# Kernel tuning notes

Hardware: AMD Instinct MI355X
Metric: run time of the kernel (lower is better)

## Reference

```python
import jax, jax.numpy as jnp
import numpy as np

D_MODEL = 1024
N_HEADS = 16
D_K = D_MODEL // N_HEADS
THETA = 10000.0
MAX_SEQ_LEN = 2048


def _rope_tables(seq_len):
    pos = jnp.arange(seq_len, dtype=jnp.float32)
    inv_freq = 1.0 / (THETA ** (jnp.arange(0, D_K, 2, dtype=jnp.float32) / D_K))
    ang = pos[:, None] * inv_freq[None, :]  # [T, D_K/2]
    return jnp.cos(ang), jnp.sin(ang)


def _apply_rope(x, cos, sin):
    # x: [..., T, D_K]; cos/sin: [T, D_K/2]
    x_even = x[..., ::2]
    x_odd = x[..., 1::2]
    r_even = x_even * cos - x_odd * sin
    r_odd = x_even * sin + x_odd * cos
    out = jnp.stack([r_even, r_odd], axis=-1)  # [..., T, D_K/2, 2]
    return out.reshape(x.shape)


def setup_inputs() -> dict:
    key = jax.random.key(0)
    ks = jax.random.split(key, 5)
    std = np.sqrt(2.0 / (D_MODEL + D_MODEL))
    x = jax.random.normal(ks[0], (2, 2048, D_MODEL), dtype=jnp.float32)
    w_q = jax.random.normal(ks[1], (D_MODEL, D_MODEL), dtype=jnp.float32) * std
    w_k = jax.random.normal(ks[2], (D_MODEL, D_MODEL), dtype=jnp.float32) * std
    w_v = jax.random.normal(ks[3], (D_MODEL, D_MODEL), dtype=jnp.float32) * std
    w_o = jax.random.normal(ks[4], (D_MODEL, D_MODEL), dtype=jnp.float32) * std
    return {"x": x, "w_q": w_q, "w_k": w_k, "w_v": w_v, "w_o": w_o}


def reference(x, w_q, w_k, w_v, w_o):
    B, T, _ = x.shape
    # projections: weight stored as [d_out, d_in], y = x @ W^T
    q = jnp.einsum('btd,od->bto', x, w_q)
    k = jnp.einsum('btd,od->bto', x, w_k)
    v = jnp.einsum('btd,od->bto', x, w_v)
    # split heads: [B, T, H*Dk] -> [B, H, T, Dk]
    q = q.reshape(B, T, N_HEADS, D_K).transpose(0, 2, 1, 3)
    k = k.reshape(B, T, N_HEADS, D_K).transpose(0, 2, 1, 3)
    v = v.reshape(B, T, N_HEADS, D_K).transpose(0, 2, 1, 3)
    cos, sin = _rope_tables(T)
    q = _apply_rope(q, cos, sin)
    k = _apply_rope(k, cos, sin)
    scores = jnp.einsum('bhqd,bhkd->bhqk', q, k) / np.sqrt(D_K).astype(np.float32)
    causal = jnp.tril(jnp.ones((T, T), dtype=bool))
    scores = jnp.where(causal, scores, -jnp.inf)
    attn = jax.nn.softmax(scores, axis=-1)
    out = jnp.einsum('bhqk,bhkd->bhqd', attn, v)
    out = out.transpose(0, 2, 1, 3).reshape(B, T, D_MODEL)
    return jnp.einsum('btd,od->bto', out, w_o)
```

## Files before the change

### kernel.cpp

```cpp
#include <hip/hip_runtime.h>
#include <hip/hip_bf16.h>

typedef __bf16 bf16_t;
typedef __bf16 bf16x8 __attribute__((ext_vector_type(8)));
typedef float f32x4 __attribute__((ext_vector_type(4)));
typedef short short4v __attribute__((ext_vector_type(4)));

#define D_MODEL 1024
#define T_SEQ 2048
#define NH 16
#define DKD 64
#define X_ELEMS (4194304u)
#define W_ELEMS (1048576u)
#define Q_SCALE 0.18033688011112042f

__device__ __forceinline__ void async16(const bf16_t* g, bf16_t* l) {
    __builtin_amdgcn_global_load_lds((const __attribute__((address_space(1))) void*)g,
                                     (__attribute__((address_space(3))) void*)l, 16, 0, 0);
}

__global__ __launch_bounds__(256) void convert_kernel(
    const float* __restrict__ x, const float* __restrict__ wq,
    const float* __restrict__ wk, const float* __restrict__ wv,
    const float* __restrict__ wo,
    bf16_t* __restrict__ xb, bf16_t* __restrict__ wqb, bf16_t* __restrict__ wkb,
    bf16_t* __restrict__ wvb, bf16_t* __restrict__ wob)
{
    size_t idx = ((size_t)blockIdx.x * 256 + threadIdx.x) * 4;
    const float* src; bf16_t* dst; size_t off;
    if (idx < X_ELEMS) { src = x; dst = xb; off = idx; }
    else {
        size_t r = idx - X_ELEMS;
        unsigned w = (unsigned)(r >> 20);
        off = r & (W_ELEMS - 1);
        src = (w == 0) ? wq : (w == 1) ? wk : (w == 2) ? wv : wo;
        dst = (w == 0) ? wqb : (w == 1) ? wkb : (w == 2) ? wvb : wob;
    }
    float4 v = *(const float4*)(src + off);
    union { bf16_t b[4]; short4v s; } u;
    u.b[0] = (bf16_t)v.x; u.b[1] = (bf16_t)v.y;
    u.b[2] = (bf16_t)v.z; u.b[3] = (bf16_t)v.w;
    *(short4v*)(dst + off) = u.s;
}

__global__ __launch_bounds__(256) void rope_kernel(float* __restrict__ cost, float* __restrict__ sint)
{
    int idx = blockIdx.x * 256 + threadIdx.x;
    int t = idx >> 5, i = idx & 31;
    float inv = expf(-0.28782313662425572f * (float)i);
    float ang = (float)t * inv;
    float s, c;
    sincosf(ang, &s, &c);
    cost[idx] = c; sint[idx] = s;
}

__device__ __forceinline__ void gemm_body(
    int mode,
    const bf16_t* __restrict__ A, const bf16_t* __restrict__ W,
    bf16_t* __restrict__ qout, bf16_t* __restrict__ kout, bf16_t* __restrict__ vout,
    const float* __restrict__ cost, const float* __restrict__ sint,
    float* __restrict__ fout)
{
    __shared__ bf16_t As[128 * 64];
    __shared__ bf16_t Bs[128 * 64];
    const int tid = threadIdx.x;
    const int wave = tid >> 6, lane = tid & 63;
    const int quad = lane >> 4, l16 = lane & 15;
    const int m0 = blockIdx.x * 128;
    const int n0 = blockIdx.y * 128;
    const int wm = (wave >> 1) * 64, wn = (wave & 1) * 64;

    const bf16_t* Afrag = (mode == 2) ? Bs : As;
    const bf16_t* Bfrag = (mode == 2) ? As : Bs;
    const int aoff = (mode == 2) ? wn : wm;
    const int boff = (mode == 2) ? wm : wn;

    const f32x4 fzero = {0.f, 0.f, 0.f, 0.f};
    f32x4 acc[4][4];
    #pragma unroll
    for (int i = 0; i < 4; ++i)
        #pragma unroll
        for (int j = 0; j < 4; ++j) acc[i][j] = fzero;

    for (int k0 = 0; k0 < 1024; k0 += 64) {
        __syncthreads();
        #pragma unroll
        for (int c = 0; c < 4; ++c) {
            int G = c * 256 + tid;
            int row = G >> 3, p = G & 7;
            int go = p ^ (row & 7);
            async16(A + (size_t)(m0 + row) * 1024 + (k0 + go * 8), As + (size_t)(c * 256 + wave * 64) * 8);
            async16(W + (size_t)(n0 + row) * 1024 + (k0 + go * 8), Bs + (size_t)(c * 256 + wave * 64) * 8);
        }
        __syncthreads();
        #pragma unroll
        for (int ks = 0; ks < 2; ++ks) {
            bf16x8 af[4], bfv[4];
            #pragma unroll
            for (int mi = 0; mi < 4; ++mi) {
                int r = aoff + mi * 16 + l16;
                af[mi] = *(const bf16x8*)(Afrag + r * 64 + (((ks * 4 + quad) ^ (r & 7)) * 8));
            }
            #pragma unroll
            for (int ni = 0; ni < 4; ++ni) {
                int r = boff + ni * 16 + l16;
                bfv[ni] = *(const bf16x8*)(Bfrag + r * 64 + (((ks * 4 + quad) ^ (r & 7)) * 8));
            }
            #pragma unroll
            for (int mi = 0; mi < 4; ++mi)
                #pragma unroll
                for (int ni = 0; ni < 4; ++ni)
                    acc[mi][ni] = __builtin_amdgcn_mfma_f32_16x16x32_bf16(af[mi], bfv[ni], acc[mi][ni], 0, 0, 0);
        }
    }

    #pragma unroll
    for (int mi = 0; mi < 4; ++mi) {
        #pragma unroll
        for (int ni = 0; ni < 4; ++ni) {
            #pragma unroll
            for (int reg = 0; reg < 4; ++reg) {
                float v = acc[mi][ni][reg];
                if (mode == 2) {
                    int f   = n0 + wn + mi * 16 + quad * 4 + reg;
                    int tok = m0 + wm + ni * 16 + l16;
                    int t = tok & (T_SEQ - 1), b = tok >> 11;
                    int h = f >> 6, dk = f & 63;
                    vout[(((size_t)b * NH + h) * DKD + dk) * T_SEQ + t] = (bf16_t)v;
                } else {
                    int row = m0 + wm + mi * 16 + quad * 4 + reg;
                    int col = n0 + wn + ni * 16 + l16;
                    if (mode == 3) {
                        fout[(size_t)row * D_MODEL + col] = v;
                    } else {
                        int t = row & (T_SEQ - 1), b = row >> 11;
                        int h = col >> 6, dk = col & 63;
                        float vp = __shfl_xor(v, 1);
                        int fi = dk >> 1;
                        float c = cost[t * 32 + fi], s = sint[t * 32 + fi];
                        float r = (dk & 1) ? (vp * s + v * c) : (v * c - vp * s);
                        if (mode == 0) r *= Q_SCALE;
                        bf16_t* dst = (mode == 0) ? qout : kout;
                        dst[(((size_t)b * NH + h) * T_SEQ + t) * DKD + dk] = (bf16_t)r;
                    }
                }
            }
        }
    }
}

__global__ __launch_bounds__(256) void gemm_qkv(
    const bf16_t* __restrict__ A,
    const bf16_t* __restrict__ W0, const bf16_t* __restrict__ W1, const bf16_t* __restrict__ W2,
    bf16_t* __restrict__ qout, bf16_t* __restrict__ kout, bf16_t* __restrict__ vout,
    const float* __restrict__ cost, const float* __restrict__ sint)
{
    const int mode = blockIdx.z;
    const bf16_t* W = (mode == 1) ? W1 : (mode == 2) ? W2 : W0;
    gemm_body(mode, A, W, qout, kout, vout, cost, sint, nullptr);
}

__global__ __launch_bounds__(256) void gemm_out(
    const bf16_t* __restrict__ A, const bf16_t* __restrict__ W,
    float* __restrict__ fout)
{
    gemm_body(3, A, W, nullptr, nullptr, nullptr, nullptr, nullptr, fout);
}

__global__ __launch_bounds__(256, 2) void attn_kernel(
    const bf16_t* __restrict__ Q, const bf16_t* __restrict__ Kb,
    const bf16_t* __restrict__ Vt, bf16_t* __restrict__ O)
{
    __shared__ float Ocomb[3][2][4][4][16][4];
    __shared__ float Lcomb[3][2][64];
    __shared__ bf16_t Pw[4][16 * 72];
    const int tid = threadIdx.x;
    const int wave = tid >> 6, lane = tid & 63;
    const int quad = lane >> 4, l16 = lane & 15;
    const int bh = blockIdx.x;
    const int qb = 63 - (int)blockIdx.y;
    const int qw = qb * 32;

    const bf16_t* kbase = Kb + (size_t)bh * T_SEQ * DKD;
    const bf16_t* vbase = Vt + (size_t)bh * DKD * T_SEQ;

    bf16x8 qf[2][2];
    #pragma unroll
    for (int j = 0; j < 2; ++j) {
        const bf16_t* qp = Q + ((size_t)bh * T_SEQ + qw + j * 16 + l16) * DKD;
        qf[j][0] = *(const bf16x8*)(qp + quad * 8);
        qf[j][1] = *(const bf16x8*)(qp + 32 + quad * 8);
    }
    const f32x4 fzero = {0.f, 0.f, 0.f, 0.f};
    f32x4 oacc[2][4];
    #pragma unroll
    for (int j = 0; j < 2; ++j)
        #pragma unroll
        for (int i = 0; i < 4; ++i) oacc[j][i] = fzero;
    float lsum[2] = {0.f, 0.f};

    const int nkt = (qw + 95) >> 6;

    bf16x8 kcur[4][2], knxt[4][2], vcur[4][2];
    #pragma unroll
    for (int fi = 0; fi < 4; ++fi) {
        const bf16_t* kr = kbase + (size_t)(wave * 64 + fi * 16 + l16) * DKD + quad * 8;
        kcur[fi][0] = *(const bf16x8*)(kr);
        kcur[fi][1] = *(const bf16x8*)(kr + 32);
    }

    for (int kt = wave; kt < nkt; kt += 4) {
        const int k0 = kt * 64;
        #pragma unroll
        for (int di = 0; di < 4; ++di) {
            const bf16_t* vr = vbase + (size_t)(di * 16 + l16) * T_SEQ + k0 + quad * 8;
            vcur[di][0] = *(const bf16x8*)(vr);
            vcur[di][1] = *(const bf16x8*)(vr + 32);
        }
        if (kt + 4 < nkt) {
            #pragma unroll
            for (int fi = 0; fi < 4; ++fi) {
                const bf16_t* kr = kbase + (size_t)((kt + 4) * 64 + fi * 16 + l16) * DKD + quad * 8;
                knxt[fi][0] = *(const bf16x8*)(kr);
                knxt[fi][1] = *(const bf16x8*)(kr + 32);
            }
        }

        #pragma unroll
        for (int j = 0; j < 2; ++j) {
            if (k0 > qw + j * 16 + 15) continue;
            const int qcol = qw + j * 16 + l16;
            f32x4 s[4];
            #pragma unroll
            for (int fi = 0; fi < 4; ++fi) {
                f32x4 z = fzero;
                z = __builtin_amdgcn_mfma_f32_16x16x32_bf16(kcur[fi][0], qf[j][0], z, 0, 0, 0);
                z = __builtin_amdgcn_mfma_f32_16x16x32_bf16(kcur[fi][1], qf[j][1], z, 0, 0, 0);
                s[fi] = z;
            }
            if (k0 + 63 > qw + j * 16) {
                #pragma unroll
                for (int fi = 0; fi < 4; ++fi)
                    #pragma unroll
                    for (int reg = 0; reg < 4; ++reg) {
                        int key = k0 + fi * 16 + quad * 4 + reg;
                        s[fi][reg] = (key > qcol) ? -__builtin_inff() : s[fi][reg];
                    }
            }
            float sm = 0.f;
            #pragma unroll
            for (int fi = 0; fi < 4; ++fi)
                #pragma unroll
                for (int reg = 0; reg < 4; ++reg) {
                    float p = __builtin_amdgcn_exp2f(s[fi][reg]);
                    s[fi][reg] = p;
                    sm += p;
                }
            lsum[j] += sm;

            bf16_t* pw = &Pw[wave][0];
            #pragma unroll
            for (int fi = 0; fi < 4; ++fi) {
                union { bf16_t h[4]; unsigned long long u64; } pk;
                pk.h[0] = (bf16_t)s[fi][0]; pk.h[1] = (bf16_t)s[fi][1];
                pk.h[2] = (bf16_t)s[fi][2]; pk.h[3] = (bf16_t)s[fi][3];
                *(unsigned long long*)(pw + l16 * 72 + fi * 16 + quad * 4) = pk.u64;
            }
            bf16x8 pf[2];
            pf[0] = *(const bf16x8*)(pw + l16 * 72 + quad * 8);
            pf[1] = *(const bf16x8*)(pw + l16 * 72 + 32 + quad * 8);

            #pragma unroll
            for (int di = 0; di < 4; ++di) {
                oacc[j][di] = __builtin_amdgcn_mfma_f32_16x16x32_bf16(vcur[di][0], pf[0], oacc[j][di], 0, 0, 0);
                oacc[j][di] = __builtin_amdgcn_mfma_f32_16x16x32_bf16(vcur[di][1], pf[1], oacc[j][di], 0, 0, 0);
            }
        }

        if (kt + 4 < nkt) {
            #pragma unroll
            for (int fi = 0; fi < 4; ++fi) {
                kcur[fi][0] = knxt[fi][0];
                kcur[fi][1] = knxt[fi][1];
            }
        }
    }

    if (wave > 0) {
        #pragma unroll
        for (int j = 0; j < 2; ++j) {
            #pragma unroll
            for (int di = 0; di < 4; ++di)
                *(f32x4*)&Ocomb[wave - 1][j][di][quad][l16][0] = oacc[j][di];
            Lcomb[wave - 1][j][lane] = lsum[j];
        }
    }
    __syncthreads();
    if (wave != 0) return;

    #pragma unroll
    for (int j = 0; j < 2; ++j) {
        #pragma unroll
        for (int w = 0; w < 3; ++w) {
            #pragma unroll
            for (int di = 0; di < 4; ++di) {
                f32x4 p = *(const f32x4*)&Ocomb[w][j][di][quad][l16][0];
                #pragma unroll
                for (int reg = 0; reg < 4; ++reg) oacc[j][di][reg] += p[reg];
            }
            lsum[j] += Lcomb[w][j][lane];
        }
    }

    const int b = bh >> 4, h = bh & 15;
    #pragma unroll
    for (int j = 0; j < 2; ++j) {
        float l = lsum[j];
        l += __shfl_xor(l, 16);
        l += __shfl_xor(l, 32);
        float rl = 1.0f / l;
        int q = qw + j * 16 + l16;
        #pragma unroll
        for (int di = 0; di < 4; ++di) {
            union { bf16_t hh[4]; unsigned long long u64; } ok;
            #pragma unroll
            for (int reg = 0; reg < 4; ++reg) ok.hh[reg] = (bf16_t)(oacc[j][di][reg] * rl);
            int d = di * 16 + quad * 4;
            *(unsigned long long*)(O + ((size_t)b * T_SEQ + q) * D_MODEL + h * DKD + d) = ok.u64;
        }
    }
}

extern "C" void kernel_launch(void* const* d_in, const int* in_sizes, int n_in,
                              void* d_out, int out_size, void* d_ws, size_t ws_size,
                              hipStream_t stream)
{
    const float* x  = (const float*)d_in[0];
    const float* wq = (const float*)d_in[1];
    const float* wk = (const float*)d_in[2];
    const float* wv = (const float*)d_in[3];
    const float* wo = (const float*)d_in[4];
    float* out = (float*)d_out;

    char* ws = (char*)d_ws;
    size_t off = 0;
    auto alloc = [&](size_t bytes) -> void* {
        void* p = ws + off; off += (bytes + 255) & ~(size_t)255; return p;
    };
    bf16_t* xb   = (bf16_t*)alloc((size_t)X_ELEMS * 2);
    bf16_t* wqb  = (bf16_t*)alloc((size_t)W_ELEMS * 2);
    bf16_t* wkb  = (bf16_t*)alloc((size_t)W_ELEMS * 2);
    bf16_t* wvb  = (bf16_t*)alloc((size_t)W_ELEMS * 2);
    bf16_t* wob  = (bf16_t*)alloc((size_t)W_ELEMS * 2);
    bf16_t* qb   = (bf16_t*)alloc((size_t)X_ELEMS * 2);
    bf16_t* kb   = (bf16_t*)alloc((size_t)X_ELEMS * 2);
    bf16_t* vtb  = (bf16_t*)alloc((size_t)X_ELEMS * 2);
    bf16_t* ob   = (bf16_t*)alloc((size_t)X_ELEMS * 2);
    float*  cost = (float*)alloc((size_t)T_SEQ * 32 * 4);
    float*  sint = (float*)alloc((size_t)T_SEQ * 32 * 4);

    convert_kernel<<<8192, 256, 0, stream>>>(x, wq, wk, wv, wo, xb, wqb, wkb, wvb, wob);
    rope_kernel<<<256, 256, 0, stream>>>(cost, sint);
    gemm_qkv<<<dim3(32, 8, 3), 256, 0, stream>>>(xb, wqb, wkb, wvb, qb, kb, vtb, cost, sint);
    attn_kernel<<<dim3(32, 64), 256, 0, stream>>>(qb, kb, vtb, ob);
    gemm_out<<<dim3(32, 8, 1), 256, 0, stream>>>(ob, wob, out);
}
```

Before: 226.6 us.

## Halve GEMM K-tile, use smaller M-tile for output projection, pack RoPE table

```diff
diff --git a/kernel.cpp b/kernel.cpp
--- a/kernel.cpp
+++ b/kernel.cpp
@@ -43,7 +43,7 @@
     *(short4v*)(dst + off) = u.s;
 }
 
-__global__ __launch_bounds__(256) void rope_kernel(float* __restrict__ cost, float* __restrict__ sint)
+__global__ __launch_bounds__(256) void rope_kernel(float2* __restrict__ ctab)
 {
     int idx = blockIdx.x * 256 + threadIdx.x;
     int t = idx >> 5, i = idx & 31;
@@ -51,24 +51,25 @@
     float ang = (float)t * inv;
     float s, c;
     sincosf(ang, &s, &c);
-    cost[idx] = c; sint[idx] = s;
-}
-
-__device__ __forceinline__ void gemm_body(
-    int mode,
-    const bf16_t* __restrict__ A, const bf16_t* __restrict__ W,
+    ctab[idx] = make_float2(c, s);
+}
+
+__global__ __launch_bounds__(256) void gemm_qkv(
+    const bf16_t* __restrict__ A,
+    const bf16_t* __restrict__ W0, const bf16_t* __restrict__ W1, const bf16_t* __restrict__ W2,
     bf16_t* __restrict__ qout, bf16_t* __restrict__ kout, bf16_t* __restrict__ vout,
-    const float* __restrict__ cost, const float* __restrict__ sint,
-    float* __restrict__ fout)
-{
-    __shared__ bf16_t As[128 * 64];
-    __shared__ bf16_t Bs[128 * 64];
+    const float2* __restrict__ ctab)
+{
+    __shared__ bf16_t As[128 * 32];
+    __shared__ bf16_t Bs[128 * 32];
     const int tid = threadIdx.x;
     const int wave = tid >> 6, lane = tid & 63;
     const int quad = lane >> 4, l16 = lane & 15;
     const int m0 = blockIdx.x * 128;
     const int n0 = blockIdx.y * 128;
     const int wm = (wave >> 1) * 64, wn = (wave & 1) * 64;
+    const int mode = blockIdx.z;
+    const bf16_t* W = (mode == 1) ? W1 : (mode == 2) ? W2 : W0;
 
     const bf16_t* Afrag = (mode == 2) ? Bs : As;
     const bf16_t* Bfrag = (mode == 2) ? As : Bs;
@@ -82,36 +83,33 @@
         #pragma unroll
         for (int j = 0; j < 4; ++j) acc[i][j] = fzero;
 
-    for (int k0 = 0; k0 < 1024; k0 += 64) {
+    for (int k0 = 0; k0 < 1024; k0 += 32) {
         __syncthreads();
         #pragma unroll
-        for (int c = 0; c < 4; ++c) {
+        for (int c = 0; c < 2; ++c) {
             int G = c * 256 + tid;
-            int row = G >> 3, p = G & 7;
-            int go = p ^ (row & 7);
+            int row = G >> 2, p = G & 3;
+            int go = p ^ ((row >> 1) & 3);
             async16(A + (size_t)(m0 + row) * 1024 + (k0 + go * 8), As + (size_t)(c * 256 + wave * 64) * 8);
             async16(W + (size_t)(n0 + row) * 1024 + (k0 + go * 8), Bs + (size_t)(c * 256 + wave * 64) * 8);
         }
         __syncthreads();
-        #pragma unroll
-        for (int ks = 0; ks < 2; ++ks) {
-            bf16x8 af[4], bfv[4];
-            #pragma unroll
-            for (int mi = 0; mi < 4; ++mi) {
-                int r = aoff + mi * 16 + l16;
-                af[mi] = *(const bf16x8*)(Afrag + r * 64 + (((ks * 4 + quad) ^ (r & 7)) * 8));
-            }
-            #pragma unroll
-            for (int ni = 0; ni < 4; ++ni) {
-                int r = boff + ni * 16 + l16;
-                bfv[ni] = *(const bf16x8*)(Bfrag + r * 64 + (((ks * 4 + quad) ^ (r & 7)) * 8));
-            }
-            #pragma unroll
-            for (int mi = 0; mi < 4; ++mi)
-                #pragma unroll
-                for (int ni = 0; ni < 4; ++ni)
-                    acc[mi][ni] = __builtin_amdgcn_mfma_f32_16x16x32_bf16(af[mi], bfv[ni], acc[mi][ni], 0, 0, 0);
-        }
+        bf16x8 af[4], bfv[4];
+        #pragma unroll
+        for (int mi = 0; mi < 4; ++mi) {
+            int r = aoff + mi * 16 + l16;
+            af[mi] = *(const bf16x8*)(Afrag + r * 32 + ((quad ^ ((r >> 1) & 3)) * 8));
+        }
+        #pragma unroll
+        for (int ni = 0; ni < 4; ++ni) {
+            int r = boff + ni * 16 + l16;
+            bfv[ni] = *(const bf16x8*)(Bfrag + r * 32 + ((quad ^ ((r >> 1) & 3)) * 8));
+        }
+        #pragma unroll
+        for (int mi = 0; mi < 4; ++mi)
+            #pragma unroll
+            for (int ni = 0; ni < 4; ++ni)
+                acc[mi][ni] = __builtin_amdgcn_mfma_f32_16x16x32_bf16(af[mi], bfv[ni], acc[mi][ni], 0, 0, 0);
     }
 
     #pragma unroll
@@ -130,41 +128,84 @@
                 } else {
                     int row = m0 + wm + mi * 16 + quad * 4 + reg;
                     int col = n0 + wn + ni * 16 + l16;
-                    if (mode == 3) {
-                        fout[(size_t)row * D_MODEL + col] = v;
-                    } else {
-                        int t = row & (T_SEQ - 1), b = row >> 11;
-                        int h = col >> 6, dk = col & 63;
-                        float vp = __shfl_xor(v, 1);
-                        int fi = dk >> 1;
-                        float c = cost[t * 32 + fi], s = sint[t * 32 + fi];
-                        float r = (dk & 1) ? (vp * s + v * c) : (v * c - vp * s);
-                        if (mode == 0) r *= Q_SCALE;
-                        bf16_t* dst = (mode == 0) ? qout : kout;
-                        dst[(((size_t)b * NH + h) * T_SEQ + t) * DKD + dk] = (bf16_t)r;
-                    }
+                    int t = row & (T_SEQ - 1), b = row >> 11;
+                    int h = col >> 6, dk = col & 63;
+                    float vp = __shfl_xor(v, 1);
+                    int fi = dk >> 1;
+                    float2 cs = ctab[t * 32 + fi];
+                    float r = (dk & 1) ? (vp * cs.y + v * cs.x) : (v * cs.x - vp * cs.y);
+                    if (mode == 0) r *= Q_SCALE;
+                    bf16_t* dst = (mode == 0) ? qout : kout;
+                    dst[(((size_t)b * NH + h) * T_SEQ + t) * DKD + dk] = (bf16_t)r;
                 }
             }
         }
     }
-}
-
-__global__ __launch_bounds__(256) void gemm_qkv(
-    const bf16_t* __restrict__ A,
-    const bf16_t* __restrict__ W0, const bf16_t* __restrict__ W1, const bf16_t* __restrict__ W2,
-    bf16_t* __restrict__ qout, bf16_t* __restrict__ kout, bf16_t* __restrict__ vout,
-    const float* __restrict__ cost, const float* __restrict__ sint)
-{
-    const int mode = blockIdx.z;
-    const bf16_t* W = (mode == 1) ? W1 : (mode == 2) ? W2 : W0;
-    gemm_body(mode, A, W, qout, kout, vout, cost, sint, nullptr);
 }
 
 __global__ __launch_bounds__(256) void gemm_out(
     const bf16_t* __restrict__ A, const bf16_t* __restrict__ W,
     float* __restrict__ fout)
 {
-    gemm_body(3, A, W, nullptr, nullptr, nullptr, nullptr, nullptr, fout);
+    __shared__ bf16_t As[64 * 32];
+    __shared__ bf16_t Bs[128 * 32];
+    const int tid = threadIdx.x;
+    const int wave = tid >> 6, lane = tid & 63;
+    const int quad = lane >> 4, l16 = lane & 15;
+    const int m0 = blockIdx.x * 64;
+    const int n0 = blockIdx.y * 128;
+    const int wm = (wave >> 1) * 32, wn = (wave & 1) * 64;
+
+    const f32x4 fzero = {0.f, 0.f, 0.f, 0.f};
+    f32x4 acc[2][4];
+    #pragma unroll
+    for (int i = 0; i < 2; ++i)
+        #pragma unroll
+        for (int j = 0; j < 4; ++j) acc[i][j] = fzero;
+
+    for (int k0 = 0; k0 < 1024; k0 += 32) {
+        __syncthreads();
+        {
+            int row = tid >> 2, p = tid & 3;
+            int go = p ^ ((row >> 1) & 3);
+            async16(A + (size_t)(m0 + row) * 1024 + (k0 + go * 8), As + (size_t)(wave * 64) * 8);
+        }
+        #pragma unroll
+        for (int c = 0; c < 2; ++c) {
+            int G = c * 256 + tid;
+            int row = G >> 2, p = G & 3;
+            int go = p ^ ((row >> 1) & 3);
+            async16(W + (size_t)(n0 + row) * 1024 + (k0 + go * 8), Bs + (size_t)(c * 256 + wave * 64) * 8);
+        }
+        __syncthreads();
+        bf16x8 af[2], bfv[4];
+        #pragma unroll
+        for (int mi = 0; mi < 2; ++mi) {
+            int r = wm + mi * 16 + l16;
+            af[mi] = *(const bf16x8*)(As + r * 32 + ((quad ^ ((r >> 1) & 3)) * 8));
+        }
+        #pragma unroll
+        for (int ni = 0; ni < 4; ++ni) {
+            int r = wn + ni * 16 + l16;
+            bfv[ni] = *(const bf16x8*)(Bs + r * 32 + ((quad ^ ((r >> 1) & 3)) * 8));
+        }
+        #pragma unroll
+        for (int mi = 0; mi < 2; ++mi)
+            #pragma unroll
+            for (int ni = 0; ni < 4; ++ni)
+                acc[mi][ni] = __builtin_amdgcn_mfma_f32_16x16x32_bf16(af[mi], bfv[ni], acc[mi][ni], 0, 0, 0);
+    }
+
+    #pragma unroll
+    for (int mi = 0; mi < 2; ++mi)
+        #pragma unroll
+        for (int ni = 0; ni < 4; ++ni)
+            #pragma unroll
+            for (int reg = 0; reg < 4; ++reg) {
+                int row = m0 + wm + mi * 16 + quad * 4 + reg;
+                int col = n0 + wn + ni * 16 + l16;
+                fout[(size_t)row * D_MODEL + col] = acc[mi][ni][reg];
+            }
 }
 
 __global__ __launch_bounds__(256, 2) void attn_kernel(
@@ -356,12 +397,11 @@
     bf16_t* kb   = (bf16_t*)alloc((size_t)X_ELEMS * 2);
     bf16_t* vtb  = (bf16_t*)alloc((size_t)X_ELEMS * 2);
     bf16_t* ob   = (bf16_t*)alloc((size_t)X_ELEMS * 2);
-    float*  cost = (float*)alloc((size_t)T_SEQ * 32 * 4);
-    float*  sint = (float*)alloc((size_t)T_SEQ * 32 * 4);
+    float2* ctab = (float2*)alloc((size_t)T_SEQ * 32 * 8);
 
     convert_kernel<<<8192, 256, 0, stream>>>(x, wq, wk, wv, wo, xb, wqb, wkb, wvb, wob);
-    rope_kernel<<<256, 256, 0, stream>>>(cost, sint);
-    gemm_qkv<<<dim3(32, 8, 3), 256, 0, stream>>>(xb, wqb, wkb, wvb, qb, kb, vtb, cost, sint);
+    rope_kernel<<<256, 256, 0, stream>>>(ctab);
+    gemm_qkv<<<dim3(32, 8, 3), 256, 0, stream>>>(xb, wqb, wkb, wvb, qb, kb, vtb, ctab);
     attn_kernel<<<dim3(32, 64), 256, 0, stream>>>(qb, kb, vtb, ob);
-    gemm_out<<<dim3(32, 8, 1), 256, 0, stream>>>(ob, wob, out);
-}
+    gemm_out<<<dim3(64, 8, 1), 256, 0, stream>>>(ob, wob, out);
+}
```

Measured after the change: 232.2 us. +2.5%, slower.
